# Kernel tuning notes

Measured on AMD Instinct MI355X. Metric: run time of the kernel, lower is better.

## Reference

```python
import jax, jax.numpy as jnp
from jax import lax
import numpy as np

B, N, CIN, COUT, HID = 16, 4096, 64, 128, 128
RATIO, K = 0.25, 32
M = int(N * RATIO)  # 1024 sampled centroids per cloud


def setup_inputs() -> dict:
    key = jax.random.key(0)
    ks = jax.random.split(key, 6)
    s = 0.02
    return {
        "x": jax.random.normal(ks[0], (B, N, CIN), jnp.float32),
        "pos": jax.random.normal(ks[1], (B, N, 3), jnp.float32),
        "W1": jax.random.normal(ks[2], (CIN + 3, HID), jnp.float32) * s,
        "b1": jnp.zeros((HID,), jnp.float32),
        "W2": jax.random.normal(ks[3], (HID, COUT), jnp.float32) * s,
        "b2": jnp.zeros((COUT,), jnp.float32),
        "Wlin": jax.random.normal(ks[4], (CIN, COUT), jnp.float32) * s,
        "blin": jnp.zeros((COUT,), jnp.float32),
    }


def mish(v):
    return v * jnp.tanh(jax.nn.softplus(v))


def fps(pc, m):
    # Farthest point sampling (deterministic start at index 0, as PyG with random_start=False).
    n = pc.shape[0]

    def step(carry, _):
        mind, last = carry
        d = jnp.sum((pc - pc[last]) ** 2, axis=-1)  # [N]
        mind = jnp.minimum(mind, d)
        nxt = jnp.argmax(mind).astype(jnp.int32)
        return (mind, nxt), nxt

    init = (jnp.full((n,), np.inf, pc.dtype), jnp.int32(0))
    _, rest = lax.scan(step, init, None, length=m - 1)
    return jnp.concatenate([jnp.zeros((1,), jnp.int32), rest])  # [M]


def reference(x, pos, W1, b1, W2, b2, Wlin, blin):
    def per_cloud(xc, pc):
        # xc: [N,CIN], pc: [N,3]
        idx = fps(pc, M)                                        # [M]
        q = pc[idx]                                             # [M,3] sampled centroids
        d2 = jnp.sum((q[:, None, :] - pc[None, :, :]) ** 2, -1)  # [M,N]
        _, nbr = lax.top_k(-d2, K)                              # [M,K] knn indices
        rel = pc[nbr] - q[:, None, :]                           # [M,K,3]
        h = jnp.concatenate([xc[nbr], rel], axis=-1)            # [M,K,CIN+3]
        h = mish(h @ W1 + b1)                                   # local_nn layer 1
        h = h @ W2 + b2                                         # [M,K,COUT]
        agg = jnp.max(h, axis=1)                                # PointNetConv max aggregation
        out = agg + xc[idx] @ Wlin + blin                       # residual skip via self.lin
        return out, q

    x_out, pos_out = jax.vmap(per_cloud)(x, pos)
    return x_out, pos_out
```

## Files before the change

kernel.cpp:

```cpp
#include <hip/hip_runtime.h>
#include <hip/hip_bf16.h>

constexpr int B    = 16;
constexpr int N    = 4096;
constexpr int CIN  = 64;
constexpr int COUT = 128;
constexpr int M    = 1024;
constexpr int K    = 32;

constexpr int K1  = 96;
constexpr int LDH = 136;

typedef __attribute__((ext_vector_type(8))) short short8;
typedef __attribute__((ext_vector_type(4))) float f32x4;
typedef __attribute__((ext_vector_type(2))) float f32x2;

static __device__ __forceinline__ unsigned short f2bf(float f) {
  unsigned u = __float_as_uint(f);
  unsigned r = (u + 0x7FFFu + ((u >> 16) & 1u)) >> 16;
  return (unsigned short)r;
}

static __device__ __forceinline__ float fast_mish(float v) {
  float u = __expf(v);
  float s = u * (u + 2.0f);
  float t = s / (s + 2.0f);
  return (v > 60.f) ? v : v * t;
}

template <int CTRL, int RM>
static __device__ __forceinline__ unsigned dpp_umax_step(unsigned x) {
  int o = __builtin_amdgcn_update_dpp((int)x, (int)x, CTRL, RM, 0xF, false);
  unsigned u = (unsigned)o;
  return x > u ? x : u;
}
static __device__ __forceinline__ unsigned wave_umax(unsigned x) {
  x = dpp_umax_step<0x111, 0xF>(x);
  x = dpp_umax_step<0x112, 0xF>(x);
  x = dpp_umax_step<0x114, 0xF>(x);
  x = dpp_umax_step<0x118, 0xF>(x);
  x = dpp_umax_step<0x142, 0xA>(x);
  x = dpp_umax_step<0x143, 0xC>(x);
  return (unsigned)__builtin_amdgcn_readlane((int)x, 63);
}

static __device__ __forceinline__ unsigned long long umax64(unsigned long long a,
                                                            unsigned long long b) {
  return a > b ? a : b;
}

__global__ __launch_bounds__(512) void fps8_kernel(const float* __restrict__ pos,
                                                   int* __restrict__ idx_out,
                                                   float* __restrict__ pout,
                                                   float* __restrict__ pos4) {
#pragma clang fp contract(off)
  const int b   = blockIdx.x;
  const int tid = threadIdx.x;
  __shared__ float sp[N][4];
  __shared__ unsigned long long skey[2][8];
  const float* p = pos + (size_t)b * (N * 3);
  float* p4 = pos4 + (size_t)b * N * 4;

  f32x2 px2[4], py2[4], pz2[4];
  float mind[8];
#pragma unroll
  for (int j = 0; j < 8; j++) {
    const int n = tid + j * 512;
    const float x = p[3 * n + 0];
    const float y = p[3 * n + 1];
    const float z = p[3 * n + 2];
    px2[j >> 1][j & 1] = x;
    py2[j >> 1][j & 1] = y;
    pz2[j >> 1][j & 1] = z;
    mind[j] = __builtin_inff();
    f32x4 v;
    v[0] = x; v[1] = y; v[2] = z; v[3] = 0.f;
    *(f32x4*)(&sp[n][0]) = v;
    *(f32x4*)(p4 + 4 * n) = v;
  }
  float qx = p[0], qy = p[1], qz = p[2];
  if (tid == 0) {
    idx_out[b * M + 0] = 0;
    pout[(size_t)(b * M + 0) * 3 + 0] = qx;
    pout[(size_t)(b * M + 0) * 3 + 1] = qy;
    pout[(size_t)(b * M + 0) * 3 + 2] = qz;
  }
  __syncthreads();

  const int wv = tid >> 6, lane = tid & 63;
  for (int t = 1; t < M; t++) {
    const f32x2 nqx = {-qx, -qx};
    const f32x2 nqy = {-qy, -qy};
    const f32x2 nqz = {-qz, -qz};
    float bv = -1.f;
    unsigned bn = 0;
#pragma unroll
    for (int k = 0; k < 4; k++) {
      f32x2 dx = px2[k] + nqx;
      f32x2 dy = py2[k] + nqy;
      f32x2 dz = pz2[k] + nqz;
      f32x2 s = (dx * dx + dy * dy) + dz * dz;
      const float mi0 = fminf(mind[2 * k + 0], s.x);
      mind[2 * k + 0] = mi0;
      bool c0 = mi0 > bv;
      bv = c0 ? mi0 : bv;
      bn = c0 ? (unsigned)(tid + (2 * k + 0) * 512) : bn;
      const float mi1 = fminf(mind[2 * k + 1], s.y);
      mind[2 * k + 1] = mi1;
      bool c1 = mi1 > bv;
      bv = c1 ? mi1 : bv;
      bn = c1 ? (unsigned)(tid + (2 * k + 1) * 512) : bn;
    }
    const unsigned vb = __float_as_uint(bv);
    const unsigned wb = wave_umax(vb);
    unsigned tk = (vb == wb) ? ~bn : 0u;
    tk = wave_umax(tk);
    const int par = t & 1;
    if (lane == 0) skey[par][wv] = ((unsigned long long)wb << 32) | tk;
    __syncthreads();
    const unsigned long long k0 = skey[par][0];
    const unsigned long long k1 = skey[par][1];
    const unsigned long long k2 = skey[par][2];
    const unsigned long long k3 = skey[par][3];
    const unsigned long long k4 = skey[par][4];
    const unsigned long long k5 = skey[par][5];
    const unsigned long long k6 = skey[par][6];
    const unsigned long long k7 = skey[par][7];
    const unsigned long long bb =
        umax64(umax64(umax64(k0, k1), umax64(k2, k3)),
               umax64(umax64(k4, k5), umax64(k6, k7)));
    const unsigned n = ~(unsigned)bb;
    const f32x4 qv = *(const f32x4*)(&sp[n][0]);
    qx = qv[0];
    qy = qv[1];
    qz = qv[2];
    if (tid == 0) {
      idx_out[b * M + t] = (int)n;
      pout[(size_t)(b * M + t) * 3 + 0] = qx;
      pout[(size_t)(b * M + t) * 3 + 1] = qy;
      pout[(size_t)(b * M + t) * 3 + 2] = qz;
    }
  }
}

__global__ __launch_bounds__(256) void prep_weights(const float* __restrict__ W1,
                                                    const float* __restrict__ W2,
                                                    unsigned short* __restrict__ W1t,
                                                    unsigned short* __restrict__ W2t) {
  const int n = blockIdx.x;
  const int t = threadIdx.x;
  if (t < K1) {
    W1t[n * K1 + t] = (t < 67) ? f2bf(W1[t * 128 + n]) : (unsigned short)0;
  } else if (t < K1 + 128) {
    int k = t - K1;
    W2t[n * 128 + k] = f2bf(W2[k * 128 + n]);
  }
}

__global__ __launch_bounds__(256) void knnmlp_kernel(
    const float* __restrict__ x, const float* __restrict__ pos4,
    const unsigned short* __restrict__ W1t, const unsigned short* __restrict__ W2t,
    const float* __restrict__ b1, const float* __restrict__ b2,
    const float* __restrict__ Wlin, const float* __restrict__ blin,
    const int* __restrict__ idx, float* __restrict__ xout) {
  __shared__ unsigned short sA2[4][32][LDH];
  const int tid  = threadIdx.x;
  const int wv   = tid >> 6;
  const int lane = tid & 63;
  const int lrow = lane & 15;
  const int g    = lane >> 4;
  unsigned short* A2 = &sA2[wv][0][0];
  const int W = blockIdx.x * 4 + wv;
  const int b = W >> 10;

  const float* p4 = pos4 + (size_t)b * N * 4;
  const int sel = idx[W];
  const f32x4 q = *(const f32x4*)(p4 + 4 * sel);
  int n0 = 0, n1 = 0;
  {
#pragma clang fp contract(off)
    const f32x2 nqx = {-q[0], -q[0]};
    const f32x2 nqy = {-q[1], -q[1]};
    const f32x2 nqz = {-q[2], -q[2]};
    float d[64];
#pragma unroll
    for (int jj = 0; jj < 32; jj++) {
      const f32x4 v0 = *(const f32x4*)(p4 + 4 * ((2 * jj + 0) * 64 + lane));
      const f32x4 v1 = *(const f32x4*)(p4 + 4 * ((2 * jj + 1) * 64 + lane));
      f32x2 vx = {v0[0], v1[0]};
      f32x2 vy = {v0[1], v1[1]};
      f32x2 vz = {v0[2], v1[2]};
      f32x2 dx = vx + nqx;
      f32x2 dy = vy + nqy;
      f32x2 dz = vz + nqz;
      f32x2 s = (dx * dx + dy * dy) + dz * dz;
      d[2 * jj + 0] = s.x;
      d[2 * jj + 1] = s.y;
    }
    float gv[8];
    int gj[8];
#pragma unroll
    for (int gg = 0; gg < 8; gg++) {
      gv[gg] = __builtin_inff();
      gj[gg] = 8 * gg;
#pragma unroll
      for (int e = 0; e < 8; e++) {
        const int j = 8 * gg + e;
        bool c = d[j] < gv[gg];
        gv[gg] = c ? d[j] : gv[gg];
        gj[gg] = c ? j : gj[gg];
      }
    }
    for (int r = 0; r < K; r++) {
      float bv = __builtin_inff();
      int bj = 0;
#pragma unroll
      for (int gg = 0; gg < 8; gg++) {
        bool c = gv[gg] < bv;
        bv = c ? gv[gg] : bv;
        bj = c ? gj[gg] : bj;
      }
      const unsigned bn = (unsigned)(bj * 64 + lane);
      const unsigned nb = ~__float_as_uint(bv);
      const unsigned wnb = wave_umax(nb);
      unsigned tk = (nb == wnb) ? (0xFFFFFFFFu - bn) : 0u;
      tk = wave_umax(tk);
      const unsigned wn = 0xFFFFFFFFu - tk;
      n0 = (r == lrow) ? (int)wn : n0;
      n1 = (r == 16 + lrow) ? (int)wn : n1;
      const int wj = (int)(wn >> 6);
      const int wl = (int)(wn & 63);
      const int wg = wj >> 3;
#pragma unroll
      for (int gg = 0; gg < 8; gg++) {
        if (gg == wg) {
#pragma unroll
          for (int e = 0; e < 8; e++) {
            if (8 * gg + e == wj) {
              if (lane == wl) d[8 * gg + e] = __builtin_inff();
            }
          }
          float nv = __builtin_inff();
          int nj = 8 * gg;
#pragma unroll
          for (int e = 0; e < 8; e++) {
            const int j = 8 * gg + e;
            bool c = d[j] < nv;
            nv = c ? d[j] : nv;
            nj = c ? j : nj;
          }
          gv[gg] = nv;
          gj[gg] = nj;
        }
      }
    }
  }

  const float qx = q[0], qy = q[1], qz = q[2];
  short8 a0[3], a1[3];
  {
    const float* xr0 = x + ((size_t)b * N + n0) * CIN;
    const float* xr1 = x + ((size_t)b * N + n1) * CIN;
#pragma unroll
    for (int kc = 0; kc < 2; kc++) {
      const int k0 = kc * 32 + g * 8;
      f32x4 u0 = *(const f32x4*)(xr0 + k0);
      f32x4 u1 = *(const f32x4*)(xr0 + k0 + 4);
      f32x4 v0 = *(const f32x4*)(xr1 + k0);
      f32x4 v1 = *(const f32x4*)(xr1 + k0 + 4);
      short8 ha, hb;
#pragma unroll
      for (int e = 0; e < 4; e++) {
        ha[e] = (short)f2bf(u0[e]);
        ha[e + 4] = (short)f2bf(u1[e]);
        hb[e] = (short)f2bf(v0[e]);
        hb[e + 4] = (short)f2bf(v1[e]);
      }
      a0[kc] = ha;
      a1[kc] = hb;
    }
    short8 z = {};
    a0[2] = z;
    a1[2] = z;
    if (g == 0) {
      float r0x = p4[4 * n0 + 0] - qx, r0y = p4[4 * n0 + 1] - qy, r0z = p4[4 * n0 + 2] - qz;
      float r1x = p4[4 * n1 + 0] - qx, r1y = p4[4 * n1 + 1] - qy, r1z = p4[4 * n1 + 2] - qz;
      a0[2][0] = (short)f2bf(r0x); a0[2][1] = (short)f2bf(r0y); a0[2][2] = (short)f2bf(r0z);
      a1[2][0] = (short)f2bf(r1x); a1[2][1] = (short)f2bf(r1y); a1[2][2] = (short)f2bf(r1z);
    }
  }

#pragma unroll 2
  for (int nt = 0; nt < 8; nt++) {
    const unsigned short* w1r = W1t + (size_t)(nt * 16 + lrow) * K1 + g * 8;
    f32x4 c0 = {}, c1 = {};
#pragma unroll
    for (int kc = 0; kc < 3; kc++) {
      short8 bfr = *(const short8*)(w1r + kc * 32);
      c0 = __builtin_amdgcn_mfma_f32_16x16x32_bf16(a0[kc], bfr, c0, 0, 0, 0);
      c1 = __builtin_amdgcn_mfma_f32_16x16x32_bf16(a1[kc], bfr, c1, 0, 0, 0);
    }
    const int colI = nt * 16 + lrow;
    const float bb = b1[colI];
#pragma unroll
    for (int reg = 0; reg < 4; reg++) {
      const int row = g * 4 + reg;
      A2[row * LDH + colI] = f2bf(fast_mish(c0[reg] + bb));
      A2[(16 + row) * LDH + colI] = f2bf(fast_mish(c1[reg] + bb));
    }
  }

  f32x4 xq[4];
  {
    const float* xs = x + ((size_t)b * N + sel) * CIN + g * 16;
#pragma unroll
    for (int v = 0; v < 4; v++) xq[v] = *(const f32x4*)(xs + 4 * v);
  }

#pragma unroll 2
  for (int nt = 0; nt < 8; nt++) {
    const unsigned short* w2r = W2t + (size_t)(nt * 16 + lrow) * 128 + g * 8;
    f32x4 c0 = {}, c1 = {};
#pragma unroll
    for (int kc = 0; kc < 4; kc++) {
      short8 af0 = *(const short8*)(A2 + lrow * LDH + kc * 32 + g * 8);
      short8 af1 = *(const short8*)(A2 + (16 + lrow) * LDH + kc * 32 + g * 8);
      short8 bfr = *(const short8*)(w2r + kc * 32);
      c0 = __builtin_amdgcn_mfma_f32_16x16x32_bf16(af0, bfr, c0, 0, 0, 0);
      c1 = __builtin_amdgcn_mfma_f32_16x16x32_bf16(af1, bfr, c1, 0, 0, 0);
    }
    float pm = fmaxf(fmaxf(fmaxf(c0[0], c0[1]), fmaxf(c0[2], c0[3])),
                     fmaxf(fmaxf(c1[0], c1[1]), fmaxf(c1[2], c1[3])));
    pm = fmaxf(pm, __shfl_xor(pm, 16, 64));
    pm = fmaxf(pm, __shfl_xor(pm, 32, 64));
    const int j = nt * 16 + lrow;
    float s = 0.f;
#pragma unroll
    for (int e = 0; e < 16; e++) {
      s += xq[e >> 2][e & 3] * Wlin[(g * 16 + e) * 128 + j];
    }
    s += __shfl_xor(s, 16, 64);
    s += __shfl_xor(s, 32, 64);
    if (g == 0) {
      xout[(size_t)W * 128 + j] = pm + b2[j] + s + blin[j];
    }
  }
}

extern "C" void kernel_launch(void* const* d_in, const int* in_sizes, int n_in,
                              void* d_out, int out_size, void* d_ws, size_t ws_size,
                              hipStream_t stream) {
  const float* x    = (const float*)d_in[0];
  const float* pos  = (const float*)d_in[1];
  const float* W1   = (const float*)d_in[2];
  const float* b1   = (const float*)d_in[3];
  const float* W2   = (const float*)d_in[4];
  const float* b2   = (const float*)d_in[5];
  const float* Wlin = (const float*)d_in[6];
  const float* blin = (const float*)d_in[7];

  float* out  = (float*)d_out;
  float* xout = out;
  float* pout = out + (size_t)B * M * COUT;

  char* ws = (char*)d_ws;
  int* idx            = (int*)ws;
  unsigned short* W1t = (unsigned short*)(ws + 65536);
  unsigned short* W2t = (unsigned short*)(ws + 90112);
  float* pos4         = (float*)(ws + 122880);

  prep_weights<<<dim3(128), dim3(256), 0, stream>>>(W1, W2, W1t, W2t);
  fps8_kernel<<<dim3(B), dim3(512), 0, stream>>>(pos, idx, pout, pos4);
  knnmlp_kernel<<<dim3(B * M / 4), dim3(256), 0, stream>>>(
      x, pos4, W1t, W2t, b1, b2, Wlin, blin, idx, xout);
}
```

Baseline: 966.0 us.

## Fuse weight prep into FPS, stage point cloud in LDS, restructure FPS argmax

Weight transposition now runs as extra blocks of the FPS kernel, which removes one launch. The FPS inner loop updates min distances with vector ops and does the argmax as a max tree followed by a first-index select, replacing the serial compare chain. The kNN/MLP kernel grows to 512 threads per block and stages the cloud's positions in shared memory so the distance scan reads LDS rather than global memory. It also swaps MFMA operands so each lane writes its hidden activations as 4-wide vectors, and computes mish with a hardware reciprocal instead of a divide. The costs are extra LDS per block, which may reduce occupancy, an added block sync, and slightly less precise mish.

```diff
diff --git a/kernel.cpp b/kernel.cpp
--- a/kernel.cpp
+++ b/kernel.cpp
@@ -12,6 +12,7 @@
 constexpr int LDH = 136;
 
 typedef __attribute__((ext_vector_type(8))) short short8;
+typedef __attribute__((ext_vector_type(4))) short short4v;
 typedef __attribute__((ext_vector_type(4))) float f32x4;
 typedef __attribute__((ext_vector_type(2))) float f32x2;
 
@@ -24,8 +25,18 @@
 static __device__ __forceinline__ float fast_mish(float v) {
   float u = __expf(v);
   float s = u * (u + 2.0f);
-  float t = s / (s + 2.0f);
+  float den = s + 2.0f;
+  float r;
+  asm("v_rcp_f32 %0, %1" : "=v"(r) : "v"(den));
+  float t = s * r;
   return (v > 60.f) ? v : v * t;
+}
+
+static __device__ __forceinline__ f32x2 fmin2(f32x2 a, f32x2 b) {
+  f32x2 r;
+  r.x = fminf(a.x, b.x);
+  r.y = fminf(a.y, b.y);
+  return r;
 }
 
 template <int CTRL, int RM>
@@ -49,11 +60,26 @@
   return a > b ? a : b;
 }
 
-__global__ __launch_bounds__(512) void fps8_kernel(const float* __restrict__ pos,
-                                                   int* __restrict__ idx_out,
-                                                   float* __restrict__ pout,
-                                                   float* __restrict__ pos4) {
+__global__ __launch_bounds__(512) void fps10_kernel(const float* __restrict__ pos,
+                                                    int* __restrict__ idx_out,
+                                                    float* __restrict__ pout,
+                                                    float* __restrict__ pos4,
+                                                    const float* __restrict__ W1,
+                                                    const float* __restrict__ W2,
+                                                    unsigned short* __restrict__ W1t,
+                                                    unsigned short* __restrict__ W2t) {
 #pragma clang fp contract(off)
+  if (blockIdx.x >= B) {
+    const int n = blockIdx.x - B;
+    const int t = threadIdx.x;
+    if (t < K1) {
+      W1t[n * K1 + t] = (t < 67) ? f2bf(W1[t * 128 + n]) : (unsigned short)0;
+    } else if (t < K1 + 128) {
+      const int k = t - K1;
+      W2t[n * 128 + k] = f2bf(W2[k * 128 + n]);
+    }
+    return;
+  }
   const int b   = blockIdx.x;
   const int tid = threadIdx.x;
   __shared__ float sp[N][4];
@@ -61,8 +87,7 @@
   const float* p = pos + (size_t)b * (N * 3);
   float* p4 = pos4 + (size_t)b * N * 4;
 
-  f32x2 px2[4], py2[4], pz2[4];
-  float mind[8];
+  f32x2 px2[4], py2[4], pz2[4], mind2[4];
 #pragma unroll
   for (int j = 0; j < 8; j++) {
     const int n = tid + j * 512;
@@ -72,7 +97,7 @@
     px2[j >> 1][j & 1] = x;
     py2[j >> 1][j & 1] = y;
     pz2[j >> 1][j & 1] = z;
-    mind[j] = __builtin_inff();
+    mind2[j >> 1][j & 1] = __builtin_inff();
     f32x4 v;
     v[0] = x; v[1] = y; v[2] = z; v[3] = 0.f;
     *(f32x4*)(&sp[n][0]) = v;
@@ -92,25 +117,28 @@
     const f32x2 nqx = {-qx, -qx};
     const f32x2 nqy = {-qy, -qy};
     const f32x2 nqz = {-qz, -qz};
-    float bv = -1.f;
-    unsigned bn = 0;
 #pragma unroll
     for (int k = 0; k < 4; k++) {
       f32x2 dx = px2[k] + nqx;
       f32x2 dy = py2[k] + nqy;
       f32x2 dz = pz2[k] + nqz;
       f32x2 s = (dx * dx + dy * dy) + dz * dz;
-      const float mi0 = fminf(mind[2 * k + 0], s.x);
-      mind[2 * k + 0] = mi0;
-      bool c0 = mi0 > bv;
-      bv = c0 ? mi0 : bv;
-      bn = c0 ? (unsigned)(tid + (2 * k + 0) * 512) : bn;
-      const float mi1 = fminf(mind[2 * k + 1], s.y);
-      mind[2 * k + 1] = mi1;
-      bool c1 = mi1 > bv;
-      bv = c1 ? mi1 : bv;
-      bn = c1 ? (unsigned)(tid + (2 * k + 1) * 512) : bn;
-    }
+      mind2[k] = fmin2(mind2[k], s);
+    }
+    const float m01 = fmaxf(fmaxf(mind2[0].x, mind2[0].y),
+                            fmaxf(mind2[1].x, mind2[1].y));
+    const float m23 = fmaxf(fmaxf(mind2[2].x, mind2[2].y),
+                            fmaxf(mind2[3].x, mind2[3].y));
+    const float bv = fmaxf(m01, m23);
+    unsigned bn = (unsigned)(tid + 7 * 512);
+    bn = (mind2[3].x == bv) ? (unsigned)(tid + 6 * 512) : bn;
+    bn = (mind2[2].y == bv) ? (unsigned)(tid + 5 * 512) : bn;
+    bn = (mind2[2].x == bv) ? (unsigned)(tid + 4 * 512) : bn;
+    bn = (mind2[1].y == bv) ? (unsigned)(tid + 3 * 512) : bn;
+    bn = (mind2[1].x == bv) ? (unsigned)(tid + 2 * 512) : bn;
+    bn = (mind2[0].y == bv) ? (unsigned)(tid + 1 * 512) : bn;
+    bn = (mind2[0].x == bv) ? (unsigned)tid : bn;
+
     const unsigned vb = __float_as_uint(bv);
     const unsigned wb = wave_umax(vb);
     unsigned tk = (vb == wb) ? ~bn : 0u;
@@ -143,50 +171,42 @@
   }
 }
 
-__global__ __launch_bounds__(256) void prep_weights(const float* __restrict__ W1,
-                                                    const float* __restrict__ W2,
-                                                    unsigned short* __restrict__ W1t,
-                                                    unsigned short* __restrict__ W2t) {
-  const int n = blockIdx.x;
-  const int t = threadIdx.x;
-  if (t < K1) {
-    W1t[n * K1 + t] = (t < 67) ? f2bf(W1[t * 128 + n]) : (unsigned short)0;
-  } else if (t < K1 + 128) {
-    int k = t - K1;
-    W2t[n * 128 + k] = f2bf(W2[k * 128 + n]);
-  }
-}
-
-__global__ __launch_bounds__(256) void knnmlp_kernel(
+__global__ __launch_bounds__(512) void knnmlp8_kernel(
     const float* __restrict__ x, const float* __restrict__ pos4,
     const unsigned short* __restrict__ W1t, const unsigned short* __restrict__ W2t,
     const float* __restrict__ b1, const float* __restrict__ b2,
     const float* __restrict__ Wlin, const float* __restrict__ blin,
     const int* __restrict__ idx, float* __restrict__ xout) {
-  __shared__ unsigned short sA2[4][32][LDH];
+  __shared__ __align__(16) unsigned char smem[8 * 32 * LDH * 2];
   const int tid  = threadIdx.x;
   const int wv   = tid >> 6;
   const int lane = tid & 63;
   const int lrow = lane & 15;
   const int g    = lane >> 4;
-  unsigned short* A2 = &sA2[wv][0][0];
-  const int W = blockIdx.x * 4 + wv;
-  const int b = W >> 10;
-
+  const int cent = blockIdx.x * 8 + wv;
+  const int b    = cent >> 10;
   const float* p4 = pos4 + (size_t)b * N * 4;
-  const int sel = idx[W];
-  const f32x4 q = *(const f32x4*)(p4 + 4 * sel);
+
+  float* sp4 = (float*)smem;
+  for (int i = tid; i < N; i += 512) {
+    *(f32x4*)(sp4 + 4 * i) = *(const f32x4*)(p4 + 4 * i);
+  }
+  __syncthreads();
+
+  const int sel = idx[cent];
+  const f32x4 q = *(const f32x4*)(sp4 + 4 * sel);
+  const float qx = q[0], qy = q[1], qz = q[2];
   int n0 = 0, n1 = 0;
   {
 #pragma clang fp contract(off)
-    const f32x2 nqx = {-q[0], -q[0]};
-    const f32x2 nqy = {-q[1], -q[1]};
-    const f32x2 nqz = {-q[2], -q[2]};
+    const f32x2 nqx = {-qx, -qx};
+    const f32x2 nqy = {-qy, -qy};
+    const f32x2 nqz = {-qz, -qz};
     float d[64];
 #pragma unroll
     for (int jj = 0; jj < 32; jj++) {
-      const f32x4 v0 = *(const f32x4*)(p4 + 4 * ((2 * jj + 0) * 64 + lane));
-      const f32x4 v1 = *(const f32x4*)(p4 + 4 * ((2 * jj + 1) * 64 + lane));
+      const f32x4 v0 = *(const f32x4*)(sp4 + 4 * ((2 * jj + 0) * 64 + lane));
+      const f32x4 v1 = *(const f32x4*)(sp4 + 4 * ((2 * jj + 1) * 64 + lane));
       f32x2 vx = {v0[0], v1[0]};
       f32x2 vy = {v0[1], v1[1]};
       f32x2 vz = {v0[2], v1[2]};
@@ -255,8 +275,10 @@
       }
     }
   }
-
-  const float qx = q[0], qy = q[1], qz = q[2];
+  __syncthreads();
+
+  unsigned short* A2 = (unsigned short*)smem + wv * (32 * LDH);
+
   short8 a0[3], a1[3];
   {
     const float* xr0 = x + ((size_t)b * N + n0) * CIN;
@@ -296,18 +318,20 @@
     f32x4 c0 = {}, c1 = {};
 #pragma unroll
     for (int kc = 0; kc < 3; kc++) {
-      short8 bfr = *(const short8*)(w1r + kc * 32);
-      c0 = __builtin_amdgcn_mfma_f32_16x16x32_bf16(a0[kc], bfr, c0, 0, 0, 0);
-      c1 = __builtin_amdgcn_mfma_f32_16x16x32_bf16(a1[kc], bfr, c1, 0, 0, 0);
-    }
-    const int colI = nt * 16 + lrow;
-    const float bb = b1[colI];
+      short8 afr = *(const short8*)(w1r + kc * 32);
+      c0 = __builtin_amdgcn_mfma_f32_16x16x32_bf16(afr, a0[kc], c0, 0, 0, 0);
+      c1 = __builtin_amdgcn_mfma_f32_16x16x32_bf16(afr, a1[kc], c1, 0, 0, 0);
+    }
+    const int kbase = nt * 16 + g * 4;
+    const f32x4 bb = *(const f32x4*)(b1 + kbase);
+    short4v h0, h1;
 #pragma unroll
     for (int reg = 0; reg < 4; reg++) {
-      const int row = g * 4 + reg;
-      A2[row * LDH + colI] = f2bf(fast_mish(c0[reg] + bb));
-      A2[(16 + row) * LDH + colI] = f2bf(fast_mish(c1[reg] + bb));
-    }
+      h0[reg] = (short)f2bf(fast_mish(c0[reg] + bb[reg]));
+      h1[reg] = (short)f2bf(fast_mish(c1[reg] + bb[reg]));
+    }
+    *(short4v*)(A2 + lrow * LDH + kbase) = h0;
+    *(short4v*)(A2 + (16 + lrow) * LDH + kbase) = h1;
   }
 
   f32x4 xq[4];
@@ -342,7 +366,7 @@
     s += __shfl_xor(s, 16, 64);
     s += __shfl_xor(s, 32, 64);
     if (g == 0) {
-      xout[(size_t)W * 128 + j] = pm + b2[j] + s + blin[j];
+      xout[(size_t)cent * 128 + j] = pm + b2[j] + s + blin[j];
     }
   }
 }
@@ -369,8 +393,8 @@
   unsigned short* W2t = (unsigned short*)(ws + 90112);
   float* pos4         = (float*)(ws + 122880);
 
-  prep_weights<<<dim3(128), dim3(256), 0, stream>>>(W1, W2, W1t, W2t);
-  fps8_kernel<<<dim3(B), dim3(512), 0, stream>>>(pos, idx, pout, pos4);
-  knnmlp_kernel<<<dim3(B * M / 4), dim3(256), 0, stream>>>(
+  fps10_kernel<<<dim3(B + 128), dim3(512), 0, stream>>>(pos, idx, pout, pos4,
+                                                        W1, W2, W1t, W2t);
+  knnmlp8_kernel<<<dim3(B * M / 8), dim3(512), 0, stream>>>(
       x, pos4, W1t, W2t, b1, b2, Wlin, blin, idx, xout);
 }
```

Result: faster. 928.2 us (-3.9%).
